# Performance work log

Measured on AMD Instinct MI355X. Metric: run time of the kernel, lower is better.

Reference implementation:

```python
import jax, jax.numpy as jnp
import numpy as np

N, V, T, C_IN, C_OUT, REL, H4, H5 = 256, 25, 128, 64, 64, 9, 18, 6


def setup_inputs() -> dict:
    key = jax.random.key(0)
    ks = jax.random.split(key, 12)

    def w(k, shape, fan_in):
        return (jax.random.normal(k, shape, jnp.float32) / np.sqrt(fan_in)).astype(jnp.float32)

    return {
        "x": jax.random.normal(ks[0], (N, V, T, C_IN), jnp.float32),
        "A": jax.random.uniform(ks[1], (V, V), dtype=jnp.float32),
        "W1": w(ks[2], (C_IN, REL), C_IN), "b1": jnp.zeros((REL,), jnp.float32),
        "W2": w(ks[3], (C_IN, REL), C_IN), "b2": jnp.zeros((REL,), jnp.float32),
        "W3": w(ks[4], (C_IN, REL), C_IN), "b3": jnp.zeros((REL,), jnp.float32),
        "W4a": w(ks[5], (REL, H4), REL), "b4a": jnp.zeros((H4,), jnp.float32),
        "W4b": w(ks[6], (H4, REL), H4), "b4b": jnp.zeros((REL,), jnp.float32),
        "W5a": w(ks[7], (REL, H5), REL), "b5a": jnp.zeros((H5,), jnp.float32),
        "W5b": w(ks[8], (H5, C_OUT), H5), "b5b": jnp.zeros((C_OUT,), jnp.float32),
    }


def reference(x, A, W1, b1, W2, b2, W3, b3, W4a, b4a, W4b, b4b, W5a, b5a, W5b, b5b):
    silu = jax.nn.silu
    alpha = 1.0
    # x: (N, V, T, C) channels-last; Linear projections to rel channels
    x1 = x @ W1 + b1                       # (N, V, T, R)
    x2 = x @ W2 + b2                       # (N, V, T, R)
    x3 = x @ W3 + b3                       # (N, V, T, R)
    # temporal mean (original: transpose(1,3).mean(-2))
    m1 = x1.mean(axis=2)                   # (N, V, R)
    m2 = x2.mean(axis=2)                   # (N, V, R)
    # pairwise joint affinity via broadcast difference
    rel = m1[:, :, None, :] - m2[:, None, :, :]   # (N, V, V, R)
    # small MLP (Linear4) on channel dim
    h = silu(rel @ W4a + b4a)              # (N, V, V, 18)
    h = silu(h @ W4b + b4b)                # (N, V, V, R)
    # scale + static adjacency (broadcast over batch and channels)
    h = h * alpha + A[None, :, :, None]    # (N, V, V, R)
    # einsum 'ncuv,nctv->nctu' in channels-last form: aggregate over v
    agg = jnp.einsum('nuvc,nvtc->nutc', h, x3)    # (N, V, T, R)
    # output MLP (Linear5)
    y = silu(agg @ W5a + b5a)              # (N, V, T, 6)
    y = silu(y @ W5b + b5b)                # (N, V, T, C_out)
    return y
```

## Files before the change

### kernel.cpp

```cpp
#include <hip/hip_runtime.h>
#include <hip/hip_fp16.h>

#define NN 256
#define VV 25
#define TT 128
#define CIN 64
#define CO 64
#define RR 9
#define HH4 18
#define HH5 6
#define TQ 16
#define NT 8

typedef unsigned int uint;

__device__ __forceinline__ float silu_f(float v) {
  return __fdividef(v, 1.0f + __expf(-v));
}
__device__ __forceinline__ __half2 u2h(uint u) {
  union { uint x; __half2 h; } c; c.x = u; return c.h;
}
__device__ __forceinline__ uint h2u(__half2 h) {
  union { __half2 h; uint x; } c; c.h = h; return c.x;
}

__global__ __launch_bounds__(128) void k1_proj(
    const float* __restrict__ x, const float* __restrict__ W3,
    const float* __restrict__ b3, uint* __restrict__ x3g,
    float* __restrict__ xm) {
  const int blk = blockIdx.x;
  const int n = blk / VV, v = blk - n * VV;
  const int tid = threadIdx.x;
  __shared__ __align__(16) __half xt[TT * 66];
  __shared__ __align__(16) float xmp[2][64];

  const float4* src = (const float4*)(x + (size_t)blk * TT * CIN);
  float4 r[16];
  #pragma unroll
  for (int k = 0; k < 16; ++k) r[k] = src[k * 128 + tid];
  #pragma unroll
  for (int k = 0; k < 16; ++k) {
    const int idx = k * 128 + tid;
    const int t = idx >> 4, c = (idx & 15) * 4;
    *(__half2*)(&xt[t * 66 + c])     = __floats2half2_rn(r[k].x, r[k].y);
    *(__half2*)(&xt[t * 66 + c + 2]) = __floats2half2_rn(r[k].z, r[k].w);
  }
  float4 cs = r[0];
  #pragma unroll
  for (int k = 1; k < 16; ++k) {
    cs.x += r[k].x; cs.y += r[k].y; cs.z += r[k].z; cs.w += r[k].w;
  }
  #pragma unroll
  for (int m = 16; m < 64; m <<= 1) {
    cs.x += __shfl_xor(cs.x, m); cs.y += __shfl_xor(cs.y, m);
    cs.z += __shfl_xor(cs.z, m); cs.w += __shfl_xor(cs.w, m);
  }
  if ((tid & 63) < 16) *(float4*)(&xmp[tid >> 6][(tid & 15) * 4]) = cs;
  __syncthreads();
  if (tid < 64) xm[(size_t)blk * 64 + tid] = xmp[0][tid] + xmp[1][tid];

  float acc[RR];
  #pragma unroll
  for (int j = 0; j < RR; ++j) acc[j] = b3[j];
  const __half* xrow = xt + tid * 66;
  #pragma unroll 8
  for (int c2 = 0; c2 < 32; ++c2) {
    const __half2 hv = *(const __half2*)(&xrow[c2 * 2]);
    const float x0 = __low2float(hv), x1 = __high2float(hv);
    #pragma unroll
    for (int j = 0; j < RR; ++j) {
      acc[j] = fmaf(x0, W3[(c2 * 2 + 0) * RR + j], acc[j]);
      acc[j] = fmaf(x1, W3[(c2 * 2 + 1) * RR + j], acc[j]);
    }
  }
  uint w[5];
  w[0] = h2u(__floats2half2_rn(acc[0], acc[1]));
  w[1] = h2u(__floats2half2_rn(acc[2], acc[3]));
  w[2] = h2u(__floats2half2_rn(acc[4], acc[5]));
  w[3] = h2u(__floats2half2_rn(acc[6], acc[7]));
  w[4] = h2u(__floats2half2_rn(acc[8], 0.f));
  const int tq = tid >> 4, t = tid & 15;
  uint* dst = x3g + (size_t)(n * NT + tq) * (5 * VV * TQ) + v * TQ + t;
  #pragma unroll
  for (int c = 0; c < 5; ++c) dst[c * (VV * TQ)] = w[c];
}

__global__ __launch_bounds__(128) void k2_h(
    const float* __restrict__ xm, const float* __restrict__ A,
    const float* __restrict__ W1, const float* __restrict__ b1,
    const float* __restrict__ W2, const float* __restrict__ b2,
    const float* __restrict__ W4a, const float* __restrict__ b4a,
    const float* __restrict__ W4b, const float* __restrict__ b4b,
    uint* __restrict__ h2g) {
  const int n = blockIdx.x;
  const int tid = threadIdx.x;
  __shared__ float m1[VV][RR + 1];
  __shared__ float m2[VV][RR + 1];
  const float* xmn = xm + (size_t)n * VV * CIN;
  for (int i = tid; i < 2 * VV * RR; i += 128) {
    const int which = (i >= VV * RR);
    const int idx = which ? i - VV * RR : i;
    const int v = idx / RR, c = idx - v * RR;
    const float* W = which ? W2 : W1;
    const float* b = which ? b2 : b1;
    const float* row = xmn + v * CIN;
    float s = 0.f;
    #pragma unroll
    for (int k = 0; k < CIN; ++k) s = fmaf(row[k], W[k * RR + c], s);
    s = s * (1.0f / TT) + b[c];
    if (which) m2[v][c] = s; else m1[v][c] = s;
  }
  __syncthreads();
  for (int p = tid; p < VV * VV; p += 128) {
    const int u = p / VV, v2 = p - u * VV;
    float rel[RR];
    #pragma unroll
    for (int j = 0; j < RR; ++j) rel[j] = m1[u][j] - m2[v2][j];
    float t1[HH4];
    #pragma unroll
    for (int k = 0; k < HH4; ++k) {
      float s = b4a[k];
      #pragma unroll
      for (int j = 0; j < RR; ++j) s = fmaf(rel[j], W4a[j * HH4 + k], s);
      t1[k] = silu_f(s);
    }
    const float av = A[u * VV + v2];
    float hc[RR];
    #pragma unroll
    for (int j = 0; j < RR; ++j) {
      float s = b4b[j];
      #pragma unroll
      for (int k = 0; k < HH4; ++k) s = fmaf(t1[k], W4b[k * RR + j], s);
      hc[j] = silu_f(s) + av;
    }
    uint* hp = h2g + (size_t)n * (VV * VV * 5) + (size_t)p * 5;
    hp[0] = h2u(__floats2half2_rn(hc[0], hc[1]));
    hp[1] = h2u(__floats2half2_rn(hc[2], hc[3]));
    hp[2] = h2u(__floats2half2_rn(hc[4], hc[5]));
    hp[3] = h2u(__floats2half2_rn(hc[6], hc[7]));
    hp[4] = h2u(__floats2half2_rn(hc[8], 0.f));
  }
}

__global__ __launch_bounds__(256) void k3_out(
    const uint* __restrict__ x3g, const uint* __restrict__ h2g,
    const float* __restrict__ W5a, const float* __restrict__ b5a,
    const float* __restrict__ W5b, const float* __restrict__ b5b,
    float* __restrict__ out) {
  const int bid = blockIdx.x;
  const int n = bid >> 3, tq = bid & 7;
  const int tid = threadIdx.x;
  __shared__ __align__(16) uint x3s[5 * VV * TQ];
  __shared__ __align__(16) uint a5s[VV * TQ * 3];

  {
    const uint4* xsrc = (const uint4*)(x3g + (size_t)bid * (5 * VV * TQ));
    for (int i = tid; i < (5 * VV * TQ) / 4; i += 256)
      ((uint4*)x3s)[i] = xsrc[i];
  }
  __syncthreads();

  for (int p = tid; p < VV * TQ; p += 256) {
    const int u = p >> 4, t = p & 15;
    const uint* hr = h2g + (size_t)n * (VV * VV * 5) + u * (VV * 5);
    const uint* xr = x3s + t;
    __half2 c0 = u2h(0u), c1 = c0, c2 = c0, c3 = c0, c4 = c0;
    #pragma unroll 5
    for (int v2 = 0; v2 < VV; ++v2) {
      const int xo = v2 * TQ;
      const uint x0 = xr[xo];
      const uint x1 = xr[xo + 400];
      const uint x2 = xr[xo + 800];
      const uint x3 = xr[xo + 1200];
      const uint x4 = xr[xo + 1600];
      const uint* hv = hr + v2 * 5;
      c0 = __hfma2(u2h(hv[0]), u2h(x0), c0);
      c1 = __hfma2(u2h(hv[1]), u2h(x1), c1);
      c2 = __hfma2(u2h(hv[2]), u2h(x2), c2);
      c3 = __hfma2(u2h(hv[3]), u2h(x3), c3);
      c4 = __hfma2(u2h(hv[4]), u2h(x4), c4);
    }
    float ag[RR];
    ag[0] = __low2float(c0); ag[1] = __high2float(c0);
    ag[2] = __low2float(c1); ag[3] = __high2float(c1);
    ag[4] = __low2float(c2); ag[5] = __high2float(c2);
    ag[6] = __low2float(c3); ag[7] = __high2float(c3);
    ag[8] = __low2float(c4);
    float a5v[HH5];
    #pragma unroll
    for (int k = 0; k < HH5; ++k) {
      float s = b5a[k];
      #pragma unroll
      for (int j = 0; j < RR; ++j) s = fmaf(ag[j], W5a[j * HH5 + k], s);
      a5v[k] = silu_f(s);
    }
    a5s[p * 3 + 0] = h2u(__floats2half2_rn(a5v[0], a5v[1]));
    a5s[p * 3 + 1] = h2u(__floats2half2_rn(a5v[2], a5v[3]));
    a5s[p * 3 + 2] = h2u(__floats2half2_rn(a5v[4], a5v[5]));
  }
  __syncthreads();

  const int cq = (tid & 15) * 4;
  float4 wb[HH5];
  #pragma unroll
  for (int k = 0; k < HH5; ++k) wb[k] = *(const float4*)(W5b + k * CO + cq);
  const float4 bb = *(const float4*)(b5b + cq);
  for (int it = 0; it < (VV * TQ) / 16; ++it) {
    const int q = it * 16 + (tid >> 4);
    const int u = q >> 4, t = q & 15;
    const __half2 p01 = u2h(a5s[q * 3 + 0]);
    const __half2 p23 = u2h(a5s[q * 3 + 1]);
    const __half2 p45 = u2h(a5s[q * 3 + 2]);
    const float a0 = __low2float(p01), a1 = __high2float(p01);
    const float a2 = __low2float(p23), a3 = __high2float(p23);
    const float a4 = __low2float(p45), a5 = __high2float(p45);
    float4 y;
    y.x = silu_f(bb.x + a0 * wb[0].x + a1 * wb[1].x + a2 * wb[2].x +
                 a3 * wb[3].x + a4 * wb[4].x + a5 * wb[5].x);
    y.y = silu_f(bb.y + a0 * wb[0].y + a1 * wb[1].y + a2 * wb[2].y +
                 a3 * wb[3].y + a4 * wb[4].y + a5 * wb[5].y);
    y.z = silu_f(bb.z + a0 * wb[0].z + a1 * wb[1].z + a2 * wb[2].z +
                 a3 * wb[3].z + a4 * wb[4].z + a5 * wb[5].z);
    y.w = silu_f(bb.w + a0 * wb[0].w + a1 * wb[1].w + a2 * wb[2].w +
                 a3 * wb[3].w + a4 * wb[4].w + a5 * wb[5].w);
    float* orow = out +
        ((size_t)(n * VV + u) * TT + tq * TQ + t) * CO + cq;
    *(float4*)orow = y;
  }
}

extern "C" void kernel_launch(void* const* d_in, const int* in_sizes, int n_in,
                              void* d_out, int out_size, void* d_ws, size_t ws_size,
                              hipStream_t stream) {
  const float* x   = (const float*)d_in[0];
  const float* A   = (const float*)d_in[1];
  const float* W1  = (const float*)d_in[2];
  const float* b1  = (const float*)d_in[3];
  const float* W2  = (const float*)d_in[4];
  const float* b2  = (const float*)d_in[5];
  const float* W3  = (const float*)d_in[6];
  const float* b3  = (const float*)d_in[7];
  const float* W4a = (const float*)d_in[8];
  const float* b4a = (const float*)d_in[9];
  const float* W4b = (const float*)d_in[10];
  const float* b4b = (const float*)d_in[11];
  const float* W5a = (const float*)d_in[12];
  const float* b5a = (const float*)d_in[13];
  const float* W5b = (const float*)d_in[14];
  const float* b5b = (const float*)d_in[15];
  float* out = (float*)d_out;

  char* ws = (char*)d_ws;
  uint*  x3g = (uint*)ws;
  float* xm  = (float*)(ws + 16384000);
  uint*  h2g = (uint*)(ws + 16384000 + 1638400);

  hipLaunchKernelGGL(k1_proj, dim3(NN * VV), dim3(128), 0, stream,
                     x, W3, b3, x3g, xm);
  hipLaunchKernelGGL(k2_h, dim3(NN), dim3(128), 0, stream,
                     xm, A, W1, b1, W2, b2, W4a, b4a, W4b, b4b, h2g);
  hipLaunchKernelGGL(k3_out, dim3(NN * NT), dim3(256), 0, stream,
                     x3g, h2g, W5a, b5a, W5b, b5b, out);
}
```

Before: 152.4 us.

## Pad x3/h intermediates to 32-byte records and read x3 directly from global

Intermediates x3 and h are now stored as padded 8-uint (32-byte) records per element, written with uint4 stores, instead of channel-planar or 5-uint packed layouts. k3 drops the LDS staging of x3 and its barrier, reading x3 and h with vector loads straight from global/cache. The second-stage buffer holds fp32 values with a stride of 7, and the output loop is reorganized per u. Padding raises workspace size and global traffic by roughly 60% for these buffers, and launch bounds request 4 blocks per CU.

```diff
diff --git a/kernel.cpp b/kernel.cpp
--- a/kernel.cpp
+++ b/kernel.cpp
@@ -73,16 +73,15 @@
       acc[j] = fmaf(x1, W3[(c2 * 2 + 1) * RR + j], acc[j]);
     }
   }
-  uint w[5];
-  w[0] = h2u(__floats2half2_rn(acc[0], acc[1]));
-  w[1] = h2u(__floats2half2_rn(acc[2], acc[3]));
-  w[2] = h2u(__floats2half2_rn(acc[4], acc[5]));
-  w[3] = h2u(__floats2half2_rn(acc[6], acc[7]));
-  w[4] = h2u(__floats2half2_rn(acc[8], 0.f));
+  uint w0 = h2u(__floats2half2_rn(acc[0], acc[1]));
+  uint w1 = h2u(__floats2half2_rn(acc[2], acc[3]));
+  uint w2 = h2u(__floats2half2_rn(acc[4], acc[5]));
+  uint w3 = h2u(__floats2half2_rn(acc[6], acc[7]));
+  uint w4 = h2u(__floats2half2_rn(acc[8], 0.f));
   const int tq = tid >> 4, t = tid & 15;
-  uint* dst = x3g + (size_t)(n * NT + tq) * (5 * VV * TQ) + v * TQ + t;
-  #pragma unroll
-  for (int c = 0; c < 5; ++c) dst[c * (VV * TQ)] = w[c];
+  uint* dst = x3g + ((((size_t)n * NT + tq) * VV + v) * TQ + t) * 8;
+  ((uint4*)dst)[0] = make_uint4(w0, w1, w2, w3);
+  ((uint4*)dst)[1] = make_uint4(w4, 0u, 0u, 0u);
 }
 
 __global__ __launch_bounds__(128) void k2_h(
@@ -133,16 +132,16 @@
       for (int k = 0; k < HH4; ++k) s = fmaf(t1[k], W4b[k * RR + j], s);
       hc[j] = silu_f(s) + av;
     }
-    uint* hp = h2g + (size_t)n * (VV * VV * 5) + (size_t)p * 5;
-    hp[0] = h2u(__floats2half2_rn(hc[0], hc[1]));
-    hp[1] = h2u(__floats2half2_rn(hc[2], hc[3]));
-    hp[2] = h2u(__floats2half2_rn(hc[4], hc[5]));
-    hp[3] = h2u(__floats2half2_rn(hc[6], hc[7]));
-    hp[4] = h2u(__floats2half2_rn(hc[8], 0.f));
-  }
-}
-
-__global__ __launch_bounds__(256) void k3_out(
+    uint* hp = h2g + ((size_t)n * (VV * VV) + p) * 8;
+    ((uint4*)hp)[0] = make_uint4(h2u(__floats2half2_rn(hc[0], hc[1])),
+                                 h2u(__floats2half2_rn(hc[2], hc[3])),
+                                 h2u(__floats2half2_rn(hc[4], hc[5])),
+                                 h2u(__floats2half2_rn(hc[6], hc[7])));
+    ((uint4*)hp)[1] = make_uint4(h2u(__floats2half2_rn(hc[8], 0.f)), 0u, 0u, 0u);
+  }
+}
+
+__global__ __launch_bounds__(256, 4) void k3_out(
     const uint* __restrict__ x3g, const uint* __restrict__ h2g,
     const float* __restrict__ W5a, const float* __restrict__ b5a,
     const float* __restrict__ W5b, const float* __restrict__ b5b,
@@ -150,35 +149,26 @@
   const int bid = blockIdx.x;
   const int n = bid >> 3, tq = bid & 7;
   const int tid = threadIdx.x;
-  __shared__ __align__(16) uint x3s[5 * VV * TQ];
-  __shared__ __align__(16) uint a5s[VV * TQ * 3];
-
-  {
-    const uint4* xsrc = (const uint4*)(x3g + (size_t)bid * (5 * VV * TQ));
-    for (int i = tid; i < (5 * VV * TQ) / 4; i += 256)
-      ((uint4*)x3s)[i] = xsrc[i];
-  }
-  __syncthreads();
+  __shared__ __align__(16) float a5s[VV * TQ * 7];
+
+  const uint* xb = x3g + (size_t)bid * (VV * TQ * 8);
 
   for (int p = tid; p < VV * TQ; p += 256) {
     const int u = p >> 4, t = p & 15;
-    const uint* hr = h2g + (size_t)n * (VV * VV * 5) + u * (VV * 5);
-    const uint* xr = x3s + t;
+    const uint* xr = xb + t * 8;
+    const uint* hr = h2g + ((size_t)n * (VV * VV) + u * VV) * 8;
     __half2 c0 = u2h(0u), c1 = c0, c2 = c0, c3 = c0, c4 = c0;
-    #pragma unroll 5
+    #pragma unroll
     for (int v2 = 0; v2 < VV; ++v2) {
-      const int xo = v2 * TQ;
-      const uint x0 = xr[xo];
-      const uint x1 = xr[xo + 400];
-      const uint x2 = xr[xo + 800];
-      const uint x3 = xr[xo + 1200];
-      const uint x4 = xr[xo + 1600];
-      const uint* hv = hr + v2 * 5;
-      c0 = __hfma2(u2h(hv[0]), u2h(x0), c0);
-      c1 = __hfma2(u2h(hv[1]), u2h(x1), c1);
-      c2 = __hfma2(u2h(hv[2]), u2h(x2), c2);
-      c3 = __hfma2(u2h(hv[3]), u2h(x3), c3);
-      c4 = __hfma2(u2h(hv[4]), u2h(x4), c4);
+      const uint4 xa = *(const uint4*)(xr + v2 * (TQ * 8));
+      const uint  xc = xr[v2 * (TQ * 8) + 4];
+      const uint4 ha = *(const uint4*)(hr + v2 * 8);
+      const uint  hc = hr[v2 * 8 + 4];
+      c0 = __hfma2(u2h(ha.x), u2h(xa.x), c0);
+      c1 = __hfma2(u2h(ha.y), u2h(xa.y), c1);
+      c2 = __hfma2(u2h(ha.z), u2h(xa.z), c2);
+      c3 = __hfma2(u2h(ha.w), u2h(xa.w), c3);
+      c4 = __hfma2(u2h(hc),   u2h(xc),   c4);
     }
     float ag[RR];
     ag[0] = __low2float(c0); ag[1] = __high2float(c0);
@@ -186,34 +176,35 @@
     ag[4] = __low2float(c2); ag[5] = __high2float(c2);
     ag[6] = __low2float(c3); ag[7] = __high2float(c3);
     ag[8] = __low2float(c4);
-    float a5v[HH5];
+    float* d = a5s + p * 7;
     #pragma unroll
     for (int k = 0; k < HH5; ++k) {
       float s = b5a[k];
       #pragma unroll
       for (int j = 0; j < RR; ++j) s = fmaf(ag[j], W5a[j * HH5 + k], s);
-      a5v[k] = silu_f(s);
-    }
-    a5s[p * 3 + 0] = h2u(__floats2half2_rn(a5v[0], a5v[1]));
-    a5s[p * 3 + 1] = h2u(__floats2half2_rn(a5v[2], a5v[3]));
-    a5s[p * 3 + 2] = h2u(__floats2half2_rn(a5v[4], a5v[5]));
-  }
-  __syncthreads();
+      d[k] = silu_f(s);
+    }
+  }
 
   const int cq = (tid & 15) * 4;
   float4 wb[HH5];
   #pragma unroll
   for (int k = 0; k < HH5; ++k) wb[k] = *(const float4*)(W5b + k * CO + cq);
   const float4 bb = *(const float4*)(b5b + cq);
-  for (int it = 0; it < (VV * TQ) / 16; ++it) {
-    const int q = it * 16 + (tid >> 4);
-    const int u = q >> 4, t = q & 15;
-    const __half2 p01 = u2h(a5s[q * 3 + 0]);
-    const __half2 p23 = u2h(a5s[q * 3 + 1]);
-    const __half2 p45 = u2h(a5s[q * 3 + 2]);
-    const float a0 = __low2float(p01), a1 = __high2float(p01);
-    const float a2 = __low2float(p23), a3 = __high2float(p23);
-    const float a4 = __low2float(p45), a5 = __high2float(p45);
+  __syncthreads();
+
+  const int t2 = tid >> 4;
+  const float* arow = a5s + t2 * 7;
+  float* obase = out +
+      (((size_t)n * VV) * TT + (size_t)tq * TQ + t2) * CO + cq;
+  #pragma unroll 5
+  for (int u = 0; u < VV; ++u) {
+    const float a0 = arow[u * 112 + 0];
+    const float a1 = arow[u * 112 + 1];
+    const float a2 = arow[u * 112 + 2];
+    const float a3 = arow[u * 112 + 3];
+    const float a4 = arow[u * 112 + 4];
+    const float a5 = arow[u * 112 + 5];
     float4 y;
     y.x = silu_f(bb.x + a0 * wb[0].x + a1 * wb[1].x + a2 * wb[2].x +
                  a3 * wb[3].x + a4 * wb[4].x + a5 * wb[5].x);
@@ -223,9 +214,7 @@
                  a3 * wb[3].z + a4 * wb[4].z + a5 * wb[5].z);
     y.w = silu_f(bb.w + a0 * wb[0].w + a1 * wb[1].w + a2 * wb[2].w +
                  a3 * wb[3].w + a4 * wb[4].w + a5 * wb[5].w);
-    float* orow = out +
-        ((size_t)(n * VV + u) * TT + tq * TQ + t) * CO + cq;
-    *(float4*)orow = y;
+    *(float4*)(obase + (size_t)u * (TT * CO)) = y;
   }
 }
 
@@ -252,8 +241,8 @@
 
   char* ws = (char*)d_ws;
   uint*  x3g = (uint*)ws;
-  float* xm  = (float*)(ws + 16384000);
-  uint*  h2g = (uint*)(ws + 16384000 + 1638400);
+  float* xm  = (float*)(ws + 26214400);
+  uint*  h2g = (uint*)(ws + 26214400 + 1638400);
 
   hipLaunchKernelGGL(k1_proj, dim3(NN * VV), dim3(128), 0, stream,
                      x, W3, b3, x3g, xm);
```

Measured after the change: 182.8 us. 1.2x slower.

## Compute joint aggregation with bf16 MFMA and padded per-channel layouts

Applied to the files above, without the earlier changes.

Replaces the packed-half2 FMA loop over joints in the output kernel with bf16 16x16x32 MFMA instructions. The h and x3 intermediates are re-laid out as per-channel bf16 tiles, with the joint dimension padded from 25 to 32 and zero-filled, and each block now covers 32 time steps instead of 16. The aim is to move the aggregation onto the matrix cores and cut VALU work. The cost is bf16 rounding in place of fp16, extra padding writes and scattered LDS transposes, and half as many blocks in the output kernel.

```diff
diff --git a/kernel.cpp b/kernel.cpp
--- a/kernel.cpp
+++ b/kernel.cpp
@@ -9,10 +9,11 @@
 #define RR 9
 #define HH4 18
 #define HH5 6
-#define TQ 16
-#define NT 8
 
 typedef unsigned int uint;
+typedef unsigned short ushort;
+typedef __attribute__((ext_vector_type(8))) short bf16x8;
+typedef __attribute__((ext_vector_type(4))) float f32x4;
 
 __device__ __forceinline__ float silu_f(float v) {
   return __fdividef(v, 1.0f + __expf(-v));
@@ -22,6 +23,11 @@
 }
 __device__ __forceinline__ uint h2u(__half2 h) {
   union { __half2 h; uint x; } c; c.h = h; return c.x;
+}
+__device__ __forceinline__ ushort f2bf(float f) {
+  union { float f; uint u; } c; c.f = f;
+  const uint u = c.u + 0x7FFFu + ((c.u >> 16) & 1u);
+  return (ushort)(u >> 16);
 }
 
 __global__ __launch_bounds__(128) void k1_proj(
@@ -29,10 +35,10 @@
     const float* __restrict__ b3, uint* __restrict__ x3g,
     float* __restrict__ xm) {
   const int blk = blockIdx.x;
-  const int n = blk / VV, v = blk - n * VV;
   const int tid = threadIdx.x;
   __shared__ __align__(16) __half xt[TT * 66];
   __shared__ __align__(16) float xmp[2][64];
+  __shared__ __align__(16) ushort ptile[RR * TT];
 
   const float4* src = (const float4*)(x + (size_t)blk * TT * CIN);
   float4 r[16];
@@ -73,16 +79,20 @@
       acc[j] = fmaf(x1, W3[(c2 * 2 + 1) * RR + j], acc[j]);
     }
   }
-  uint w[5];
-  w[0] = h2u(__floats2half2_rn(acc[0], acc[1]));
-  w[1] = h2u(__floats2half2_rn(acc[2], acc[3]));
-  w[2] = h2u(__floats2half2_rn(acc[4], acc[5]));
-  w[3] = h2u(__floats2half2_rn(acc[6], acc[7]));
-  w[4] = h2u(__floats2half2_rn(acc[8], 0.f));
-  const int tq = tid >> 4, t = tid & 15;
-  uint* dst = x3g + (size_t)(n * NT + tq) * (5 * VV * TQ) + v * TQ + t;
-  #pragma unroll
-  for (int c = 0; c < 5; ++c) dst[c * (VV * TQ)] = w[c];
+  #pragma unroll
+  for (int j = 0; j < RR; ++j) ptile[j * TT + tid] = f2bf(acc[j]);
+  __syncthreads();
+
+  const uint* tu = (const uint*)ptile;
+  uint* dst = x3g + (size_t)blk * 576;
+  #pragma unroll
+  for (int it = 0; it < 5; ++it) {
+    const int i = it * 128 + tid;
+    if (i < 576) {
+      const int c = i >> 6, tp = i & 63;
+      dst[(tp >> 4) * 144 + c * 16 + (tp & 15)] = tu[i];
+    }
+  }
 }
 
 __global__ __launch_bounds__(128) void k2_h(
@@ -91,7 +101,7 @@
     const float* __restrict__ W2, const float* __restrict__ b2,
     const float* __restrict__ W4a, const float* __restrict__ b4a,
     const float* __restrict__ W4b, const float* __restrict__ b4b,
-    uint* __restrict__ h2g) {
+    ushort* __restrict__ h2g) {
   const int n = blockIdx.x;
   const int tid = threadIdx.x;
   __shared__ float m1[VV][RR + 1];
@@ -110,6 +120,11 @@
     s = s * (1.0f / TT) + b[c];
     if (which) m2[v][c] = s; else m1[v][c] = s;
   }
+  ushort* hb = h2g + (size_t)n * (RR * 1024);
+  for (int i = tid; i < RR * 1024; i += 128) {
+    const int uv = i & 1023;
+    if ((uv >> 5) >= VV || (uv & 31) >= VV) hb[i] = 0;
+  }
   __syncthreads();
   for (int p = tid; p < VV * VV; p += 128) {
     const int u = p / VV, v2 = p - u * VV;
@@ -125,89 +140,90 @@
       t1[k] = silu_f(s);
     }
     const float av = A[u * VV + v2];
-    float hc[RR];
     #pragma unroll
     for (int j = 0; j < RR; ++j) {
       float s = b4b[j];
       #pragma unroll
       for (int k = 0; k < HH4; ++k) s = fmaf(t1[k], W4b[k * RR + j], s);
-      hc[j] = silu_f(s) + av;
-    }
-    uint* hp = h2g + (size_t)n * (VV * VV * 5) + (size_t)p * 5;
-    hp[0] = h2u(__floats2half2_rn(hc[0], hc[1]));
-    hp[1] = h2u(__floats2half2_rn(hc[2], hc[3]));
-    hp[2] = h2u(__floats2half2_rn(hc[4], hc[5]));
-    hp[3] = h2u(__floats2half2_rn(hc[6], hc[7]));
-    hp[4] = h2u(__floats2half2_rn(hc[8], 0.f));
-  }
-}
-
-__global__ __launch_bounds__(256) void k3_out(
-    const uint* __restrict__ x3g, const uint* __restrict__ h2g,
+      hb[j * 1024 + u * 32 + v2] = f2bf(silu_f(s) + av);
+    }
+  }
+}
+
+__global__ __launch_bounds__(256, 4) void k3_out(
+    const uint* __restrict__ x3g, const ushort* __restrict__ h2g,
     const float* __restrict__ W5a, const float* __restrict__ b5a,
     const float* __restrict__ W5b, const float* __restrict__ b5b,
     float* __restrict__ out) {
   const int bid = blockIdx.x;
-  const int n = bid >> 3, tq = bid & 7;
+  const int n = bid >> 2, th = bid & 3;
   const int tid = threadIdx.x;
-  __shared__ __align__(16) uint x3s[5 * VV * TQ];
-  __shared__ __align__(16) uint a5s[VV * TQ * 3];
-
-  {
-    const uint4* xsrc = (const uint4*)(x3g + (size_t)bid * (5 * VV * TQ));
-    for (int i = tid; i < (5 * VV * TQ) / 4; i += 256)
-      ((uint4*)x3s)[i] = xsrc[i];
-  }
-  __syncthreads();
-
-  for (int p = tid; p < VV * TQ; p += 256) {
-    const int u = p >> 4, t = p & 15;
-    const uint* hr = h2g + (size_t)n * (VV * VV * 5) + u * (VV * 5);
-    const uint* xr = x3s + t;
-    __half2 c0 = u2h(0u), c1 = c0, c2 = c0, c3 = c0, c4 = c0;
-    #pragma unroll 5
-    for (int v2 = 0; v2 < VV; ++v2) {
-      const int xo = v2 * TQ;
-      const uint x0 = xr[xo];
-      const uint x1 = xr[xo + 400];
-      const uint x2 = xr[xo + 800];
-      const uint x3 = xr[xo + 1200];
-      const uint x4 = xr[xo + 1600];
-      const uint* hv = hr + v2 * 5;
-      c0 = __hfma2(u2h(hv[0]), u2h(x0), c0);
-      c1 = __hfma2(u2h(hv[1]), u2h(x1), c1);
-      c2 = __hfma2(u2h(hv[2]), u2h(x2), c2);
-      c3 = __hfma2(u2h(hv[3]), u2h(x3), c3);
-      c4 = __hfma2(u2h(hv[4]), u2h(x4), c4);
-    }
-    float ag[RR];
-    ag[0] = __low2float(c0); ag[1] = __high2float(c0);
-    ag[2] = __low2float(c1); ag[3] = __high2float(c1);
-    ag[4] = __low2float(c2); ag[5] = __high2float(c2);
-    ag[6] = __low2float(c3); ag[7] = __high2float(c3);
-    ag[8] = __low2float(c4);
-    float a5v[HH5];
-    #pragma unroll
-    for (int k = 0; k < HH5; ++k) {
-      float s = b5a[k];
-      #pragma unroll
-      for (int j = 0; j < RR; ++j) s = fmaf(ag[j], W5a[j * HH5 + k], s);
-      a5v[k] = silu_f(s);
-    }
-    a5s[p * 3 + 0] = h2u(__floats2half2_rn(a5v[0], a5v[1]));
-    a5s[p * 3 + 1] = h2u(__floats2half2_rn(a5v[2], a5v[3]));
-    a5s[p * 3 + 2] = h2u(__floats2half2_rn(a5v[4], a5v[5]));
-  }
-  __syncthreads();
-
+  __shared__ __align__(16) ushort xlds[RR * 32 * 40];
+  __shared__ __align__(16) uint a5s[VV * 32 * 3];
+
+  const uint* srcu = x3g + (size_t)n * (VV * 576) + th * 144;
+  for (int i = tid; i < VV * 144; i += 256) {
+    const int v = i / 144, r = i - v * 144;
+    const uint w = srcu[v * 576 + r];
+    const int c = r >> 4, tpl = r & 15;
+    const int base = c * 1280 + (tpl * 2) * 40 + v;
+    xlds[base]      = (ushort)(w & 0xffffu);
+    xlds[base + 40] = (ushort)(w >> 16);
+  }
+  for (int i = tid; i < RR * 32 * 7; i += 256) {
+    const int c = i / 224, r2 = i - c * 224;
+    const int t = r2 / 7, v = 25 + (r2 - t * 7);
+    xlds[c * 1280 + t * 40 + v] = 0;
+  }
   const int cq = (tid & 15) * 4;
   float4 wb[HH5];
   #pragma unroll
   for (int k = 0; k < HH5; ++k) wb[k] = *(const float4*)(W5b + k * CO + cq);
   const float4 bb = *(const float4*)(b5b + cq);
-  for (int it = 0; it < (VV * TQ) / 16; ++it) {
+  __syncthreads();
+
+  const int wid = tid >> 6, lane = tid & 63;
+  const int nt = wid & 1, mt = wid >> 1;
+  const int lr = lane & 15, kb = lane >> 4;
+  const int tl = nt * 16 + lr;
+
+  bf16x8 Bf[RR];
+  #pragma unroll
+  for (int c = 0; c < RR; ++c)
+    Bf[c] = *(const bf16x8*)(xlds + c * 1280 + tl * 40 + kb * 8);
+
+  const ushort* hbase = h2g + (size_t)n * (RR * 1024) + (mt * 16 + lr) * 32 + kb * 8;
+  f32x4 acc[RR];
+  #pragma unroll
+  for (int c = 0; c < RR; ++c) {
+    const bf16x8 Af = *(const bf16x8*)(hbase + c * 1024);
+    f32x4 z = {0.f, 0.f, 0.f, 0.f};
+    acc[c] = __builtin_amdgcn_mfma_f32_16x16x32_bf16(Af, Bf[c], z, 0, 0, 0);
+  }
+
+  #pragma unroll
+  for (int j = 0; j < 4; ++j) {
+    const int u = mt * 16 + kb * 4 + j;
+    if (u < VV) {
+      float a5v[HH5];
+      #pragma unroll
+      for (int k = 0; k < HH5; ++k) {
+        float s = b5a[k];
+        #pragma unroll
+        for (int c = 0; c < RR; ++c) s = fmaf(acc[c][j], W5a[c * HH5 + k], s);
+        a5v[k] = silu_f(s);
+      }
+      uint* d = a5s + (u * 32 + tl) * 3;
+      d[0] = h2u(__floats2half2_rn(a5v[0], a5v[1]));
+      d[1] = h2u(__floats2half2_rn(a5v[2], a5v[3]));
+      d[2] = h2u(__floats2half2_rn(a5v[4], a5v[5]));
+    }
+  }
+  __syncthreads();
+
+  for (int it = 0; it < 50; ++it) {
     const int q = it * 16 + (tid >> 4);
-    const int u = q >> 4, t = q & 15;
+    const int u = q >> 5, tl2 = q & 31;
     const __half2 p01 = u2h(a5s[q * 3 + 0]);
     const __half2 p23 = u2h(a5s[q * 3 + 1]);
     const __half2 p45 = u2h(a5s[q * 3 + 2]);
@@ -224,7 +240,7 @@
     y.w = silu_f(bb.w + a0 * wb[0].w + a1 * wb[1].w + a2 * wb[2].w +
                  a3 * wb[3].w + a4 * wb[4].w + a5 * wb[5].w);
     float* orow = out +
-        ((size_t)(n * VV + u) * TT + tq * TQ + t) * CO + cq;
+        (((size_t)(n * VV + u)) * TT + th * 32 + tl2) * CO + cq;
     *(float4*)orow = y;
   }
 }
@@ -251,14 +267,14 @@
   float* out = (float*)d_out;
 
   char* ws = (char*)d_ws;
-  uint*  x3g = (uint*)ws;
-  float* xm  = (float*)(ws + 16384000);
-  uint*  h2g = (uint*)(ws + 16384000 + 1638400);
+  uint*   x3g = (uint*)ws;
+  float*  xm  = (float*)(ws + 14745600);
+  ushort* h2g = (ushort*)(ws + 16384000);
 
   hipLaunchKernelGGL(k1_proj, dim3(NN * VV), dim3(128), 0, stream,
                      x, W3, b3, x3g, xm);
   hipLaunchKernelGGL(k2_h, dim3(NN), dim3(128), 0, stream,
                      xm, A, W1, b1, W2, b2, W4a, b4a, W4b, b4b, h2g);
-  hipLaunchKernelGGL(k3_out, dim3(NN * NT), dim3(256), 0, stream,
+  hipLaunchKernelGGL(k3_out, dim3(NN * 4), dim3(256), 0, stream,
                      x3g, h2g, W5a, b5a, W5b, b5b, out);
 }
```

New measurement: 160.3 us. 5.2% more time.
